# Kernel optimization log

Hardware: AMD Instinct MI355X
Metric: run time of the kernel (lower is better)

## Reference

```python
import jax, jax.numpy as jnp
import numpy as np

QMIN, QMAX = -128.0, 127.0


def setup_inputs() -> dict:
    key = jax.random.key(0)
    kx, kw, kb = jax.random.split(key, 3)
    B, S, K, M = 4, 2048, 4096, 4096
    x = jax.random.normal(kx, (B, S, K), dtype=jnp.float32)
    bound = 1.0 / np.sqrt(K)  # kaiming_uniform(a=sqrt(5)) -> U(-1/sqrt(fan_in), 1/sqrt(fan_in))
    W = jax.random.uniform(kw, (M, K), dtype=jnp.float32, minval=-bound, maxval=bound)
    b = jax.random.uniform(kb, (M,), dtype=jnp.float32, minval=-bound, maxval=bound)
    return {"x": x, "W": W, "b": b}


def _quant_weights_rowwise(W):
    # symmetric per-row int8: scale = absmax/127
    absmax = jnp.max(jnp.abs(W), axis=1, keepdims=True)  # [M,1]
    scale = jnp.where(absmax > 0, absmax / QMAX, 1.0)
    Wq = jnp.clip(jnp.round(W / scale), QMIN, QMAX)
    return Wq, scale


def _quant_acts_per_token(X):
    # asymmetric per-token (per column of X.t()) int8 with zero-point
    xmin = jnp.min(X, axis=1, keepdims=True)  # [N,1]
    xmax = jnp.max(X, axis=1, keepdims=True)
    rng = xmax - xmin
    scale = jnp.where(rng > 0, rng / (QMAX - QMIN), 1.0)
    zp = jnp.clip(jnp.round(QMIN - xmin / scale), QMIN, QMAX)
    Xq = jnp.clip(jnp.round(X / scale + zp), QMIN, QMAX)
    return Xq, scale, zp


def reference(x, W, b):
    B, S, K = x.shape
    X = x.reshape(-1, K)  # [N, K]
    Wq, row_scale = _quant_weights_rowwise(W)          # [M,K], [M,1]
    Xq, col_scale, zp = _quant_acts_per_token(X)       # [N,K], [N,1], [N,1]
    # fused dequant-GEMM: Y = ((Xq - zp) * col_scale) @ (Wq * row_scale).T
    Wdq = Wq * row_scale                               # [M,K]
    Xdq = (Xq - zp) * col_scale                        # [N,K]
    Y = jnp.einsum('nk,mk->nm', Xdq, Wdq) + b          # [N,M]
    return Y.reshape(B, S, -1)
```

## Files before the change

kernel.cpp:

```cpp
#include <hip/hip_runtime.h>
#include <stdint.h>


typedef __attribute__((ext_vector_type(4))) int int4v;

__device__ __forceinline__ void async_load16(const void* g, void* l) {
    __builtin_amdgcn_global_load_lds(
        (const __attribute__((address_space(1))) void*)g,
        (__attribute__((address_space(3))) void*)l, 16, 0, 0);
}

__device__ __forceinline__ int quant_clip(float v) {
    return (int)fminf(fmaxf(rintf(v), -128.f), 127.f);
}

__global__ __launch_bounds__(256) void wquant_kernel(
    const float* __restrict__ W, int8_t* __restrict__ Wq,
    float* __restrict__ row_scale, int* __restrict__ wsum, int K) {
    const int row  = blockIdx.x;
    const int tid  = threadIdx.x;
    const int lane = tid & 63;
    const int wv   = tid >> 6;

    const float4* w4 = (const float4*)(W + (size_t)row * K);
    float4 vals[4];
    float amax = 0.f;
#pragma unroll
    for (int i = 0; i < 4; ++i) {
        float4 v = w4[tid + i * 256];
        vals[i] = v;
        amax = fmaxf(amax, fmaxf(fmaxf(fabsf(v.x), fabsf(v.y)),
                                 fmaxf(fabsf(v.z), fabsf(v.w))));
    }
#pragma unroll
    for (int off = 32; off > 0; off >>= 1)
        amax = fmaxf(amax, __shfl_down(amax, off, 64));

    __shared__ float smax[4];
    __shared__ int   isum[4];
    if (lane == 0) smax[wv] = amax;
    __syncthreads();
    amax = fmaxf(fmaxf(smax[0], smax[1]), fmaxf(smax[2], smax[3]));

    const float scale = (amax > 0.f) ? (amax / 127.f) : 1.f;

    int ssum = 0;
    int* wq32 = (int*)(Wq + (size_t)row * K);
#pragma unroll
    for (int i = 0; i < 4; ++i) {
        float4 v = vals[i];
        int q0 = quant_clip(v.x / scale);
        int q1 = quant_clip(v.y / scale);
        int q2 = quant_clip(v.z / scale);
        int q3 = quant_clip(v.w / scale);
        ssum += q0 + q1 + q2 + q3;
        wq32[tid + i * 256] =
            (q0 & 0xff) | ((q1 & 0xff) << 8) | ((q2 & 0xff) << 16) | ((q3 & 0xff) << 24);
    }
#pragma unroll
    for (int off = 32; off > 0; off >>= 1)
        ssum += __shfl_down(ssum, off, 64);
    if (lane == 0) isum[wv] = ssum;
    __syncthreads();
    if (tid == 0) {
        wsum[row] = isum[0] + isum[1] + isum[2] + isum[3];
        row_scale[row] = scale;
    }
}

__global__ __launch_bounds__(256) void xquant_kernel(
    const float* __restrict__ X, int8_t* __restrict__ Xq,
    float* __restrict__ col_scale, int* __restrict__ zp, int K) {
    const int row  = blockIdx.x;
    const int tid  = threadIdx.x;
    const int lane = tid & 63;
    const int wv   = tid >> 6;

    const float4* x4 = (const float4*)(X + (size_t)row * K);
    float4 vals[4];
    float vmin = 3.402823466e+38f, vmax = -3.402823466e+38f;
#pragma unroll
    for (int i = 0; i < 4; ++i) {
        float4 v = x4[tid + i * 256];
        vals[i] = v;
        vmin = fminf(vmin, fminf(fminf(v.x, v.y), fminf(v.z, v.w)));
        vmax = fmaxf(vmax, fmaxf(fmaxf(v.x, v.y), fmaxf(v.z, v.w)));
    }
#pragma unroll
    for (int off = 32; off > 0; off >>= 1) {
        vmin = fminf(vmin, __shfl_down(vmin, off, 64));
        vmax = fmaxf(vmax, __shfl_down(vmax, off, 64));
    }
    __shared__ float smin[4], smax[4];
    if (lane == 0) { smin[wv] = vmin; smax[wv] = vmax; }
    __syncthreads();
    vmin = fminf(fminf(smin[0], smin[1]), fminf(smin[2], smin[3]));
    vmax = fmaxf(fmaxf(smax[0], smax[1]), fmaxf(smax[2], smax[3]));

    const float rng   = vmax - vmin;
    const float scale = (rng > 0.f) ? (rng / 255.f) : 1.f;
    const float zpf   = fminf(fmaxf(rintf(-128.f - vmin / scale), -128.f), 127.f);

    int* xq32 = (int*)(Xq + (size_t)row * K);
#pragma unroll
    for (int i = 0; i < 4; ++i) {
        float4 v = vals[i];
        int q0 = quant_clip(v.x / scale + zpf);
        int q1 = quant_clip(v.y / scale + zpf);
        int q2 = quant_clip(v.z / scale + zpf);
        int q3 = quant_clip(v.w / scale + zpf);
        xq32[tid + i * 256] =
            (q0 & 0xff) | ((q1 & 0xff) << 8) | ((q2 & 0xff) << 16) | ((q3 & 0xff) << 24);
    }
    if (tid == 0) {
        col_scale[row] = scale;
        zp[row] = (int)zpf;
    }
}

#define TBK 64

__global__ __launch_bounds__(256) void gemm_i8_kernel(
    const int8_t* __restrict__ Xq, const int8_t* __restrict__ Wq,
    const float* __restrict__ cs, const int* __restrict__ zp,
    const float* __restrict__ rs, const int* __restrict__ wsum,
    const float* __restrict__ bias, float* __restrict__ out,
    int N, int M, int K) {
    __shared__ __align__(16) int8_t As[128 * TBK];
    __shared__ __align__(16) int8_t Bs[128 * TBK];

    const int t    = threadIdx.x;
    const int wv   = t >> 6;
    const int lane = t & 63;
    const int r    = lane & 15;
    const int qd   = lane >> 4;

    const int m0 = blockIdx.x * 128;
    const int n0 = blockIdx.y * 128;
    const int wn = (wv >> 1) * 64;
    const int wm = (wv & 1) * 64;

    int4v acc[4][4];
#pragma unroll
    for (int i = 0; i < 4; ++i)
#pragma unroll
        for (int j = 0; j < 4; ++j)
            acc[i][j] = (int4v)(0);

    const int c0 = t, c1 = 256 + t;
    const size_t gA0 = (size_t)(n0 + (c0 >> 2)) * K + (c0 & 3) * 16;
    const size_t gA1 = (size_t)(n0 + (c1 >> 2)) * K + (c1 & 3) * 16;
    const size_t gB0 = (size_t)(m0 + (c0 >> 2)) * K + (c0 & 3) * 16;
    const size_t gB1 = (size_t)(m0 + (c1 >> 2)) * K + (c1 & 3) * 16;
    int8_t* lA0 = As + wv * 1024;
    int8_t* lA1 = As + 4096 + wv * 1024;
    int8_t* lB0 = Bs + wv * 1024;
    int8_t* lB1 = Bs + 4096 + wv * 1024;

    for (int k0 = 0; k0 < K; k0 += TBK) {
        async_load16(Xq + gA0 + k0, lA0);
        async_load16(Xq + gA1 + k0, lA1);
        async_load16(Wq + gB0 + k0, lB0);
        async_load16(Wq + gB1 + k0, lB1);
        __syncthreads();

        int4v a[4], b[4];
#pragma unroll
        for (int i = 0; i < 4; ++i)
            a[i] = *(const int4v*)(As + (wn + i * 16 + r) * TBK + qd * 16);
#pragma unroll
        for (int j = 0; j < 4; ++j)
            b[j] = *(const int4v*)(Bs + (wm + j * 16 + r) * TBK + qd * 16);

#pragma unroll
        for (int i = 0; i < 4; ++i)
#pragma unroll
            for (int j = 0; j < 4; ++j)
                acc[i][j] = __builtin_amdgcn_mfma_i32_16x16x64_i8(
                    a[i], b[j], acc[i][j], 0, 0, 0);
        __syncthreads();
    }

#pragma unroll
    for (int j = 0; j < 4; ++j) {
        const int m = m0 + wm + j * 16 + r;
        const float rsm = rs[m];
        const float bm  = bias[m];
        const int   wsm = wsum[m];
#pragma unroll
        for (int i = 0; i < 4; ++i) {
            const int nb = n0 + wn + i * 16 + qd * 4;
#pragma unroll
            for (int v = 0; v < 4; ++v) {
                const int n = nb + v;
                const int ival = acc[i][j][v] - zp[n] * wsm;
                out[(size_t)n * M + m] = cs[n] * rsm * (float)ival + bm;
            }
        }
    }
}

extern "C" void kernel_launch(void* const* d_in, const int* in_sizes, int n_in,
                              void* d_out, int out_size, void* d_ws, size_t ws_size,
                              hipStream_t stream) {
    const float* x = (const float*)d_in[0];
    const float* W = (const float*)d_in[1];
    const float* b = (const float*)d_in[2];
    float* out = (float*)d_out;

    const int M = in_sizes[2];
    const int K = in_sizes[1] / M;
    const int N = in_sizes[0] / K;

    int8_t* Xq = (int8_t*)d_ws;
    int8_t* Wq = Xq + (size_t)N * K;
    float* cs  = (float*)(Wq + (size_t)M * K);
    int* zps   = (int*)(cs + N);
    float* rs  = (float*)(zps + N);
    int* wsum  = (int*)(rs + M);

    wquant_kernel<<<dim3(M), dim3(256), 0, stream>>>(W, Wq, rs, wsum, K);
    xquant_kernel<<<dim3(N), dim3(256), 0, stream>>>(x, Xq, cs, zps, K);
    gemm_i8_kernel<<<dim3(M / 128, N / 128), dim3(256), 0, stream>>>(
        Xq, Wq, cs, zps, rs, wsum, b, out, N, M, K);
}
```

Before: 478.3 us.

## Use 32x32x32 int8 MFMA with swizzled LDS and merge quant kernels

Switches the GEMM from 16x16x64 int8 MFMA tiles to 32x32x32 int8 MFMA with 16-register accumulators. It adds an XOR swizzle on the 16-byte chunk index in LDS to reduce bank conflicts on fragment reads. The two quantization kernels are merged into one launch, and the per-element divisions become multiplication by a reciprocal. Multiplying by a reciprocal can round differently from the reference division, and the epilogue's store pattern also changes.

```diff
diff --git a/kernel.cpp b/kernel.cpp
--- a/kernel.cpp
+++ b/kernel.cpp
@@ -2,7 +2,8 @@
 #include <stdint.h>
 
 
-typedef __attribute__((ext_vector_type(4))) int int4v;
+typedef __attribute__((ext_vector_type(4)))  int int4v;
+typedef __attribute__((ext_vector_type(16))) int int16v;
 
 __device__ __forceinline__ void async_load16(const void* g, void* l) {
     __builtin_amdgcn_global_load_lds(
@@ -14,111 +15,106 @@
     return (int)fminf(fmaxf(rintf(v), -128.f), 127.f);
 }
 
-__global__ __launch_bounds__(256) void wquant_kernel(
-    const float* __restrict__ W, int8_t* __restrict__ Wq,
-    float* __restrict__ row_scale, int* __restrict__ wsum, int K) {
-    const int row  = blockIdx.x;
+__global__ __launch_bounds__(256) void quant_kernel(
+    const float* __restrict__ W, const float* __restrict__ X,
+    int8_t* __restrict__ Wq, int8_t* __restrict__ Xq,
+    float* __restrict__ row_scale, int* __restrict__ wsum,
+    float* __restrict__ col_scale, int* __restrict__ zp, int M, int K) {
+    const int blk  = blockIdx.x;
     const int tid  = threadIdx.x;
     const int lane = tid & 63;
     const int wv   = tid >> 6;
-
-    const float4* w4 = (const float4*)(W + (size_t)row * K);
-    float4 vals[4];
-    float amax = 0.f;
-#pragma unroll
-    for (int i = 0; i < 4; ++i) {
-        float4 v = w4[tid + i * 256];
-        vals[i] = v;
-        amax = fmaxf(amax, fmaxf(fmaxf(fabsf(v.x), fabsf(v.y)),
-                                 fmaxf(fabsf(v.z), fabsf(v.w))));
-    }
-#pragma unroll
-    for (int off = 32; off > 0; off >>= 1)
-        amax = fmaxf(amax, __shfl_down(amax, off, 64));
-
-    __shared__ float smax[4];
+    __shared__ float sred0[4], sred1[4];
     __shared__ int   isum[4];
-    if (lane == 0) smax[wv] = amax;
-    __syncthreads();
-    amax = fmaxf(fmaxf(smax[0], smax[1]), fmaxf(smax[2], smax[3]));
-
-    const float scale = (amax > 0.f) ? (amax / 127.f) : 1.f;
-
-    int ssum = 0;
-    int* wq32 = (int*)(Wq + (size_t)row * K);
-#pragma unroll
-    for (int i = 0; i < 4; ++i) {
-        float4 v = vals[i];
-        int q0 = quant_clip(v.x / scale);
-        int q1 = quant_clip(v.y / scale);
-        int q2 = quant_clip(v.z / scale);
-        int q3 = quant_clip(v.w / scale);
-        ssum += q0 + q1 + q2 + q3;
-        wq32[tid + i * 256] =
-            (q0 & 0xff) | ((q1 & 0xff) << 8) | ((q2 & 0xff) << 16) | ((q3 & 0xff) << 24);
-    }
-#pragma unroll
-    for (int off = 32; off > 0; off >>= 1)
-        ssum += __shfl_down(ssum, off, 64);
-    if (lane == 0) isum[wv] = ssum;
-    __syncthreads();
-    if (tid == 0) {
-        wsum[row] = isum[0] + isum[1] + isum[2] + isum[3];
-        row_scale[row] = scale;
-    }
-}
-
-__global__ __launch_bounds__(256) void xquant_kernel(
-    const float* __restrict__ X, int8_t* __restrict__ Xq,
-    float* __restrict__ col_scale, int* __restrict__ zp, int K) {
-    const int row  = blockIdx.x;
-    const int tid  = threadIdx.x;
-    const int lane = tid & 63;
-    const int wv   = tid >> 6;
-
-    const float4* x4 = (const float4*)(X + (size_t)row * K);
-    float4 vals[4];
-    float vmin = 3.402823466e+38f, vmax = -3.402823466e+38f;
-#pragma unroll
-    for (int i = 0; i < 4; ++i) {
-        float4 v = x4[tid + i * 256];
-        vals[i] = v;
-        vmin = fminf(vmin, fminf(fminf(v.x, v.y), fminf(v.z, v.w)));
-        vmax = fmaxf(vmax, fmaxf(fmaxf(v.x, v.y), fmaxf(v.z, v.w)));
-    }
-#pragma unroll
-    for (int off = 32; off > 0; off >>= 1) {
-        vmin = fminf(vmin, __shfl_down(vmin, off, 64));
-        vmax = fmaxf(vmax, __shfl_down(vmax, off, 64));
-    }
-    __shared__ float smin[4], smax[4];
-    if (lane == 0) { smin[wv] = vmin; smax[wv] = vmax; }
-    __syncthreads();
-    vmin = fminf(fminf(smin[0], smin[1]), fminf(smin[2], smin[3]));
-    vmax = fmaxf(fmaxf(smax[0], smax[1]), fmaxf(smax[2], smax[3]));
-
-    const float rng   = vmax - vmin;
-    const float scale = (rng > 0.f) ? (rng / 255.f) : 1.f;
-    const float zpf   = fminf(fmaxf(rintf(-128.f - vmin / scale), -128.f), 127.f);
-
-    int* xq32 = (int*)(Xq + (size_t)row * K);
-#pragma unroll
-    for (int i = 0; i < 4; ++i) {
-        float4 v = vals[i];
-        int q0 = quant_clip(v.x / scale + zpf);
-        int q1 = quant_clip(v.y / scale + zpf);
-        int q2 = quant_clip(v.z / scale + zpf);
-        int q3 = quant_clip(v.w / scale + zpf);
-        xq32[tid + i * 256] =
-            (q0 & 0xff) | ((q1 & 0xff) << 8) | ((q2 & 0xff) << 16) | ((q3 & 0xff) << 24);
-    }
-    if (tid == 0) {
-        col_scale[row] = scale;
-        zp[row] = (int)zpf;
-    }
-}
-
-#define TBK 64
+
+    if (blk < M) {
+        const int row = blk;
+        const float4* w4 = (const float4*)(W + (size_t)row * K);
+        float4 vals[4];
+        float amax = 0.f;
+#pragma unroll
+        for (int i = 0; i < 4; ++i) {
+            float4 v = w4[tid + i * 256];
+            vals[i] = v;
+            amax = fmaxf(amax, fmaxf(fmaxf(fabsf(v.x), fabsf(v.y)),
+                                     fmaxf(fabsf(v.z), fabsf(v.w))));
+        }
+#pragma unroll
+        for (int off = 32; off > 0; off >>= 1)
+            amax = fmaxf(amax, __shfl_down(amax, off, 64));
+        if (lane == 0) sred0[wv] = amax;
+        __syncthreads();
+        amax = fmaxf(fmaxf(sred0[0], sred0[1]), fmaxf(sred0[2], sred0[3]));
+
+        const float scale = (amax > 0.f) ? (amax / 127.f) : 1.f;
+        const float inv   = 1.f / scale;
+
+        int ssum = 0;
+        int* wq32 = (int*)(Wq + (size_t)row * K);
+#pragma unroll
+        for (int i = 0; i < 4; ++i) {
+            float4 v = vals[i];
+            int q0 = quant_clip(v.x * inv);
+            int q1 = quant_clip(v.y * inv);
+            int q2 = quant_clip(v.z * inv);
+            int q3 = quant_clip(v.w * inv);
+            ssum += q0 + q1 + q2 + q3;
+            wq32[tid + i * 256] =
+                (q0 & 0xff) | ((q1 & 0xff) << 8) | ((q2 & 0xff) << 16) | ((q3 & 0xff) << 24);
+        }
+#pragma unroll
+        for (int off = 32; off > 0; off >>= 1)
+            ssum += __shfl_down(ssum, off, 64);
+        if (lane == 0) isum[wv] = ssum;
+        __syncthreads();
+        if (tid == 0) {
+            wsum[row] = isum[0] + isum[1] + isum[2] + isum[3];
+            row_scale[row] = scale;
+        }
+    } else {
+        const int row = blk - M;
+        const float4* x4 = (const float4*)(X + (size_t)row * K);
+        float4 vals[4];
+        float vmin = 3.402823466e+38f, vmax = -3.402823466e+38f;
+#pragma unroll
+        for (int i = 0; i < 4; ++i) {
+            float4 v = x4[tid + i * 256];
+            vals[i] = v;
+            vmin = fminf(vmin, fminf(fminf(v.x, v.y), fminf(v.z, v.w)));
+            vmax = fmaxf(vmax, fmaxf(fmaxf(v.x, v.y), fmaxf(v.z, v.w)));
+        }
+#pragma unroll
+        for (int off = 32; off > 0; off >>= 1) {
+            vmin = fminf(vmin, __shfl_down(vmin, off, 64));
+            vmax = fmaxf(vmax, __shfl_down(vmax, off, 64));
+        }
+        if (lane == 0) { sred0[wv] = vmin; sred1[wv] = vmax; }
+        __syncthreads();
+        vmin = fminf(fminf(sred0[0], sred0[1]), fminf(sred0[2], sred0[3]));
+        vmax = fmaxf(fmaxf(sred1[0], sred1[1]), fmaxf(sred1[2], sred1[3]));
+
+        const float rng   = vmax - vmin;
+        const float scale = (rng > 0.f) ? (rng / 255.f) : 1.f;
+        const float inv   = 1.f / scale;
+        const float zpf   = fminf(fmaxf(rintf(-128.f - vmin * inv), -128.f), 127.f);
+
+        int* xq32 = (int*)(Xq + (size_t)row * K);
+#pragma unroll
+        for (int i = 0; i < 4; ++i) {
+            float4 v = vals[i];
+            int q0 = quant_clip(v.x * inv + zpf);
+            int q1 = quant_clip(v.y * inv + zpf);
+            int q2 = quant_clip(v.z * inv + zpf);
+            int q3 = quant_clip(v.w * inv + zpf);
+            xq32[tid + i * 256] =
+                (q0 & 0xff) | ((q1 & 0xff) << 8) | ((q2 & 0xff) << 16) | ((q3 & 0xff) << 24);
+        }
+        if (tid == 0) {
+            col_scale[row] = scale;
+            zp[row] = (int)zpf;
+        }
+    }
+}
 
 __global__ __launch_bounds__(256) void gemm_i8_kernel(
     const int8_t* __restrict__ Xq, const int8_t* __restrict__ Wq,
@@ -126,75 +122,99 @@
     const float* __restrict__ rs, const int* __restrict__ wsum,
     const float* __restrict__ bias, float* __restrict__ out,
     int N, int M, int K) {
-    __shared__ __align__(16) int8_t As[128 * TBK];
-    __shared__ __align__(16) int8_t Bs[128 * TBK];
+    __shared__ __align__(16) int8_t As[128 * 64];
+    __shared__ __align__(16) int8_t Bs[128 * 64];
 
     const int t    = threadIdx.x;
     const int wv   = t >> 6;
     const int lane = t & 63;
-    const int r    = lane & 15;
-    const int qd   = lane >> 4;
+    const int r32  = lane & 31;
+    const int half = lane >> 5;
 
     const int m0 = blockIdx.x * 128;
     const int n0 = blockIdx.y * 128;
     const int wn = (wv >> 1) * 64;
     const int wm = (wv & 1) * 64;
 
-    int4v acc[4][4];
-#pragma unroll
-    for (int i = 0; i < 4; ++i)
-#pragma unroll
-        for (int j = 0; j < 4; ++j)
-            acc[i][j] = (int4v)(0);
-
-    const int c0 = t, c1 = 256 + t;
-    const size_t gA0 = (size_t)(n0 + (c0 >> 2)) * K + (c0 & 3) * 16;
-    const size_t gA1 = (size_t)(n0 + (c1 >> 2)) * K + (c1 & 3) * 16;
-    const size_t gB0 = (size_t)(m0 + (c0 >> 2)) * K + (c0 & 3) * 16;
-    const size_t gB1 = (size_t)(m0 + (c1 >> 2)) * K + (c1 & 3) * 16;
+    int16v acc[2][2];
+#pragma unroll
+    for (int i = 0; i < 2; ++i)
+#pragma unroll
+        for (int j = 0; j < 2; ++j)
+            acc[i][j] = (int16v)(0);
+
+    const int r0 = t >> 2;
+    const int c0 = (t & 3) ^ ((r0 >> 1) & 3);
+    const size_t gA0 = (size_t)(n0 + r0) * K + c0 * 16;
+    const size_t gA1 = (size_t)(n0 + 64 + r0) * K + c0 * 16;
+    const size_t gB0 = (size_t)(m0 + r0) * K + c0 * 16;
+    const size_t gB1 = (size_t)(m0 + 64 + r0) * K + c0 * 16;
     int8_t* lA0 = As + wv * 1024;
     int8_t* lA1 = As + 4096 + wv * 1024;
     int8_t* lB0 = Bs + wv * 1024;
     int8_t* lB1 = Bs + 4096 + wv * 1024;
 
-    for (int k0 = 0; k0 < K; k0 += TBK) {
+    int abase[2], bbase[2], asw[2], bsw[2];
+#pragma unroll
+    for (int i = 0; i < 2; ++i) {
+        const int ra = wn + i * 32 + r32;
+        abase[i] = ra * 64;
+        asw[i]   = (ra >> 1) & 3;
+        const int rb = wm + i * 32 + r32;
+        bbase[i] = rb * 64;
+        bsw[i]   = (rb >> 1) & 3;
+    }
+
+    for (int k0 = 0; k0 < K; k0 += 64) {
         async_load16(Xq + gA0 + k0, lA0);
         async_load16(Xq + gA1 + k0, lA1);
         async_load16(Wq + gB0 + k0, lB0);
         async_load16(Wq + gB1 + k0, lB1);
         __syncthreads();
 
-        int4v a[4], b[4];
-#pragma unroll
-        for (int i = 0; i < 4; ++i)
-            a[i] = *(const int4v*)(As + (wn + i * 16 + r) * TBK + qd * 16);
-#pragma unroll
-        for (int j = 0; j < 4; ++j)
-            b[j] = *(const int4v*)(Bs + (wm + j * 16 + r) * TBK + qd * 16);
-
-#pragma unroll
-        for (int i = 0; i < 4; ++i)
-#pragma unroll
-            for (int j = 0; j < 4; ++j)
-                acc[i][j] = __builtin_amdgcn_mfma_i32_16x16x64_i8(
-                    a[i], b[j], acc[i][j], 0, 0, 0);
-        __syncthreads();
-    }
-
-#pragma unroll
-    for (int j = 0; j < 4; ++j) {
-        const int m = m0 + wm + j * 16 + r;
-        const float rsm = rs[m];
-        const float bm  = bias[m];
-        const int   wsm = wsum[m];
-#pragma unroll
-        for (int i = 0; i < 4; ++i) {
-            const int nb = n0 + wn + i * 16 + qd * 4;
-#pragma unroll
-            for (int v = 0; v < 4; ++v) {
-                const int n = nb + v;
-                const int ival = acc[i][j][v] - zp[n] * wsm;
-                out[(size_t)n * M + m] = cs[n] * rsm * (float)ival + bm;
+        int4v a[2][2], b[2][2];
+#pragma unroll
+        for (int s = 0; s < 2; ++s) {
+            const int ch = s * 2 + half;
+#pragma unroll
+            for (int i = 0; i < 2; ++i) {
+                a[s][i] = *(const int4v*)(As + abase[i] + ((ch ^ asw[i]) << 4));
+                b[s][i] = *(const int4v*)(Bs + bbase[i] + ((ch ^ bsw[i]) << 4));
+            }
+        }
+#pragma unroll
+        for (int s = 0; s < 2; ++s)
+#pragma unroll
+            for (int i = 0; i < 2; ++i)
+#pragma unroll
+                for (int j = 0; j < 2; ++j)
+                    acc[i][j] = __builtin_amdgcn_mfma_i32_32x32x32_i8(
+                        a[s][i], b[s][j], acc[i][j], 0, 0, 0);
+        __syncthreads();
+    }
+
+    int   mm[2];
+    float rsv[2], bv[2];
+    int   wsv[2];
+#pragma unroll
+    for (int j = 0; j < 2; ++j) {
+        mm[j]  = m0 + wm + j * 32 + r32;
+        rsv[j] = rs[mm[j]];
+        bv[j]  = bias[mm[j]];
+        wsv[j] = wsum[mm[j]];
+    }
+#pragma unroll
+    for (int i = 0; i < 2; ++i) {
+        const int nb = n0 + wn + i * 32 + half * 4;
+#pragma unroll
+        for (int reg = 0; reg < 16; ++reg) {
+            const int n = nb + (reg & 3) + 8 * (reg >> 2);
+            const float csn = cs[n];
+            const int   zpn = zp[n];
+#pragma unroll
+            for (int j = 0; j < 2; ++j) {
+                const int ival = acc[i][j][reg] - zpn * wsv[j];
+                out[(size_t)n * M + mm[j]] = csn * rsv[j] * (float)ival + bv[j];
             }
         }
     }
@@ -219,8 +239,8 @@
     float* rs  = (float*)(zps + N);
     int* wsum  = (int*)(rs + M);
 
-    wquant_kernel<<<dim3(M), dim3(256), 0, stream>>>(W, Wq, rs, wsum, K);
-    xquant_kernel<<<dim3(N), dim3(256), 0, stream>>>(x, Xq, cs, zps, K);
+    quant_kernel<<<dim3(M + N), dim3(256), 0, stream>>>(
+        W, x, Wq, Xq, rs, wsum, cs, zps, M, K);
     gemm_i8_kernel<<<dim3(M / 128, N / 128), dim3(256), 0, stream>>>(
         Xq, Wq, cs, zps, rs, wsum, b, out, N, M, K);
 }
```

New measurement: 443.3 us. 7.3% less time.
